# Kernel tuning notes

Hardware: AMD Instinct MI355X
Metric: run time of the kernel (lower is better)

The kernel has to match this reference:

```python
import jax, jax.numpy as jnp
import numpy as np

N_NODE = 50000
N_EDGE = 1600000
D_NODE = 64
D_EDGE = 32
D_OUT = 32
D_IN = 2 * D_NODE + D_EDGE  # 160
D_HID = 2 * D_IN            # 320


def setup_inputs() -> dict:
    key = jax.random.key(0)
    k = jax.random.split(key, 8)
    nodes = jax.random.normal(k[0], (N_NODE, D_NODE), dtype=jnp.float32)
    edges = jax.random.normal(k[1], (N_EDGE, D_EDGE), dtype=jnp.float32)
    senders = jax.random.randint(k[2], (N_EDGE,), 0, N_NODE, dtype=jnp.int64)
    receivers = jax.random.randint(k[3], (N_EDGE,), 0, N_NODE, dtype=jnp.int64)
    # Kaiming-ish scaled linear weights
    W1 = jax.random.normal(k[4], (D_IN, D_HID), dtype=jnp.float32) / np.sqrt(D_IN)
    b1 = jnp.zeros((D_HID,), dtype=jnp.float32)
    W2 = jax.random.normal(k[5], (D_HID, D_OUT), dtype=jnp.float32) / np.sqrt(D_HID)
    b2 = jnp.zeros((D_OUT,), dtype=jnp.float32)
    return {"nodes": nodes, "edges": edges, "senders": senders,
            "receivers": receivers, "W1": W1, "b1": b1, "W2": W2, "b2": b2}


def reference(nodes, edges, senders, receivers, W1, b1, W2, b2):
    # gather sender/receiver node feats, concat with edge feats: [n_edge, 2*d_node+d_edge]
    feats = jnp.concatenate([nodes[senders], nodes[receivers], edges], axis=-1)
    h = jax.nn.sigmoid(feats @ W1 + b1)   # [n_edge, 2*d]
    new_edges = h @ W2 + b2               # [n_edge, d_edge_out]
    return new_edges
```

## Files before the change

### kernel.cpp

```cpp
#include <hip/hip_runtime.h>

typedef unsigned short u16;
typedef short bf8 __attribute__((ext_vector_type(8)));
typedef float f4 __attribute__((ext_vector_type(4)));

#define N_EDGE   1600000
#define NTILE    50000
#define BLOCKS   256
#define WAVES    12
#define NTHREADS (WAVES * 64)
#define SLOTS    (BLOCKS * WAVES)

#define WS_W2_OFF   51200
#define WS_B1_OFF   61440
#define WS_STATIC_B 124160
#define SMEM_INT4   7760

__device__ __forceinline__ u16 f2bf(float x) {
  union { float f; unsigned u; } v; v.f = x;
  unsigned r = v.u + 0x7FFFu + ((v.u >> 16) & 1u);
  return (u16)(r >> 16);
}

__device__ __forceinline__ unsigned pk2(float lo, float hi) {
  unsigned r;
  asm("v_cvt_pk_bf16_f32 %0, %1, %2" : "=v"(r) : "v"(lo), "v"(hi));
  return r;
}

union bfu { uint4 u; bf8 v; };

__device__ __forceinline__ bf8 cvt8r(const float* __restrict__ s) {
  const float4 v0 = *(const float4*)s;
  const float4 v1 = *(const float4*)(s + 4);
  bfu o;
  o.u.x = pk2(v0.x, v0.y); o.u.y = pk2(v0.z, v0.w);
  o.u.z = pk2(v1.x, v1.y); o.u.w = pk2(v1.z, v1.w);
  return o.v;
}

__device__ __forceinline__ bf8 cvt8r_nt(const float* __restrict__ s) {
  const f4 v0 = __builtin_nontemporal_load((const f4*)s);
  const f4 v1 = __builtin_nontemporal_load((const f4*)(s + 4));
  bfu o;
  o.u.x = pk2(v0[0], v0[1]); o.u.y = pk2(v0[2], v0[3]);
  o.u.z = pk2(v1[0], v1[1]); o.u.w = pk2(v1[2], v1[3]);
  return o.v;
}

__global__ void prep_kernel(const float* __restrict__ nodes,
                            const float* __restrict__ W1,
                            const float* __restrict__ b1,
                            const float* __restrict__ W2,
                            u16* __restrict__ w1t,
                            u16* __restrict__ w2t,
                            float* __restrict__ b1t,
                            u16* __restrict__ nodes_bf) {
  const int b = blockIdx.x, t = threadIdx.x;
  if (b < 200) {
    const int i = b * 256 + t;
    const int j = i & 7, lane = (i >> 3) & 63, f = i >> 9;
    const int kk = f % 5, sub = (f / 5) & 1, p = f / 10;
    const int g = lane >> 4, l15 = lane & 15;
    const int k = 32 * kk + 8 * g + j;
    const int hcol = 32 * p + 8 * (l15 >> 2) + 4 * sub + (l15 & 3);
    w1t[i] = f2bf(-1.44269504f * W1[k * 320 + hcol]);
  } else if (b < 240) {
    const int i = (b - 200) * 256 + t;
    const int j = i & 7, lane = (i >> 3) & 63, f = i >> 9;
    const int am = f & 1, p = f >> 1;
    const int g = lane >> 4, l15 = lane & 15;
    w2t[i] = f2bf(W2[(32 * p + 8 * g + j) * 32 + 16 * am + l15]);
  } else if (b == 240) {
    for (int i = t; i < 320; i += 256) {
      const int af = i >> 4, row = i & 15;
      const int hcol = 32 * (af >> 1) + 8 * (row >> 2) + 4 * (af & 1) + (row & 3);
      b1t[i] = -1.44269504f * b1[hcol];
    }
  } else {
    const int i = (b - 241) * 256 + t;
    const float4 v = ((const float4*)nodes)[i];
    ushort4 o;
    o.x = f2bf(v.x); o.y = f2bf(v.y); o.z = f2bf(v.z); o.w = f2bf(v.w);
    ((ushort4*)nodes_bf)[i] = o;
  }
}

__launch_bounds__(NTHREADS, 3)
__global__ void edge_mlp(const float* __restrict__ edges,
                         const int*   __restrict__ senders,
                         const int*   __restrict__ receivers,
                         const float* __restrict__ nodes_f,
                         const u16*   __restrict__ nodes_bf,
                         const int4*  __restrict__ wsrc,
                         const float* __restrict__ b2,
                         float* __restrict__ out,
                         int use_bf) {
  __shared__ __align__(16) int4 smem4[SMEM_INT4];
  const u16*   w1s = (const u16*)smem4;
  const u16*   w2s = w1s + WS_W2_OFF;
  const float* b1s = (const float*)(w1s + WS_B1_OFF);

  for (int i = threadIdx.x; i < SMEM_INT4; i += NTHREADS) smem4[i] = wsrc[i];
  __syncthreads();

  const int tid = threadIdx.x;
  const int lane = tid & 63;
  const int wid  = tid >> 6;
  const int l15  = lane & 15;
  const int g    = lane >> 4;

  f4 b2v[2];
  b2v[0] = *(const f4*)(b2 + 4 * g);
  b2v[1] = *(const f4*)(b2 + 16 + 4 * g);

  for (int t = blockIdx.x * WAVES + wid; t < NTILE; t += SLOTS) {
    const int e0 = t * 32;

    int es[2], er[2];
    es[0] = senders[e0 + l15];        es[1] = senders[e0 + 16 + l15];
    er[0] = receivers[e0 + l15];      er[1] = receivers[e0 + 16 + l15];

    bf8 bf[5][2];
    #pragma unroll
    for (int ef = 0; ef < 2; ++ef) {
      if (use_bf) {
        const u16* sb = nodes_bf + es[ef] * 64;
        const u16* rb = nodes_bf + er[ef] * 64;
        bf[0][ef] = *(const bf8*)(sb + 8 * g);
        bf[1][ef] = *(const bf8*)(sb + 32 + 8 * g);
        bf[2][ef] = *(const bf8*)(rb + 8 * g);
        bf[3][ef] = *(const bf8*)(rb + 32 + 8 * g);
      } else {
        const float* sb = nodes_f + es[ef] * 64;
        const float* rb = nodes_f + er[ef] * 64;
        bf[0][ef] = cvt8r(sb + 8 * g);
        bf[1][ef] = cvt8r(sb + 32 + 8 * g);
        bf[2][ef] = cvt8r(rb + 8 * g);
        bf[3][ef] = cvt8r(rb + 32 + 8 * g);
      }
      bf[4][ef] = cvt8r_nt(edges + (e0 + 16 * ef + l15) * 32 + 8 * g);
    }

    f4 acc2[2][2];
    acc2[0][0] = b2v[0]; acc2[0][1] = b2v[0];
    acc2[1][0] = b2v[1]; acc2[1][1] = b2v[1];

    #pragma unroll 2
    for (int p = 0; p < 10; ++p) {
      f4 h[2][2];
      #pragma unroll
      for (int sub = 0; sub < 2; ++sub) {
        const int af = 2 * p + sub;
        const f4 binit = *(const f4*)(b1s + af * 16 + 4 * g);
        h[sub][0] = binit;
        h[sub][1] = binit;
        #pragma unroll
        for (int kk = 0; kk < 5; ++kk) {
          const bf8 a = *(const bf8*)(w1s + ((p * 10 + sub * 5 + kk) * 64 + lane) * 8);
          h[sub][0] = __builtin_amdgcn_mfma_f32_16x16x32_bf16(a, bf[kk][0], h[sub][0], 0, 0, 0);
          h[sub][1] = __builtin_amdgcn_mfma_f32_16x16x32_bf16(a, bf[kk][1], h[sub][1], 0, 0, 0);
        }
      }
      bf8 pb[2];
      #pragma unroll
      for (int ef = 0; ef < 2; ++ef) {
        f4 s0, s1;
        #pragma unroll
        for (int r = 0; r < 4; ++r) {
          s0[r] = __builtin_amdgcn_rcpf(1.0f + __builtin_amdgcn_exp2f(h[0][ef][r]));
          s1[r] = __builtin_amdgcn_rcpf(1.0f + __builtin_amdgcn_exp2f(h[1][ef][r]));
        }
        bfu o;
        o.u.x = pk2(s0[0], s0[1]); o.u.y = pk2(s0[2], s0[3]);
        o.u.z = pk2(s1[0], s1[1]); o.u.w = pk2(s1[2], s1[3]);
        pb[ef] = o.v;
      }
      #pragma unroll
      for (int am = 0; am < 2; ++am) {
        const bf8 wa = *(const bf8*)(w2s + ((p * 2 + am) * 64 + lane) * 8);
        acc2[am][0] = __builtin_amdgcn_mfma_f32_16x16x32_bf16(wa, pb[0], acc2[am][0], 0, 0, 0);
        acc2[am][1] = __builtin_amdgcn_mfma_f32_16x16x32_bf16(wa, pb[1], acc2[am][1], 0, 0, 0);
      }
    }

    #pragma unroll
    for (int am = 0; am < 2; ++am)
      #pragma unroll
      for (int ef = 0; ef < 2; ++ef)
        __builtin_nontemporal_store(acc2[am][ef],
            (f4*)(out + (e0 + 16 * ef + l15) * 32 + 16 * am + 4 * g));
  }
}

extern "C" void kernel_launch(void* const* d_in, const int* in_sizes, int n_in,
                              void* d_out, int out_size, void* d_ws, size_t ws_size,
                              hipStream_t stream) {
  const float* nodes     = (const float*)d_in[0];
  const float* edges     = (const float*)d_in[1];
  const int*   senders   = (const int*)d_in[2];
  const int*   receivers = (const int*)d_in[3];
  const float* W1        = (const float*)d_in[4];
  const float* b1        = (const float*)d_in[5];
  const float* W2        = (const float*)d_in[6];
  const float* b2        = (const float*)d_in[7];
  float* out             = (float*)d_out;

  u16*   w1t      = (u16*)d_ws;
  u16*   w2t      = w1t + WS_W2_OFF;
  float* b1t      = (float*)(w1t + WS_B1_OFF);
  u16*   nodes_bf = (u16*)((char*)d_ws + WS_STATIC_B);
  const int use_bf = (ws_size >= (size_t)(WS_STATIC_B + 6400000)) ? 1 : 0;

  const int prep_blocks = use_bf ? (241 + 3125) : 241;
  prep_kernel<<<prep_blocks, 256, 0, stream>>>(nodes, W1, b1, W2, w1t, w2t, b1t, nodes_bf);
  edge_mlp<<<BLOCKS, NTHREADS, 0, stream>>>(edges, senders, receivers, nodes, nodes_bf,
                                            (const int4*)d_ws, b2, out, use_bf);
}
```

Measured before the change: 231.4 us.

## Software-pipeline layer-1 MFMA with sigmoid/layer-2 and use library bf16 convert

Restructures the hidden-chunk loop into a two-stage software pipeline. The next chunk's layer-1 MFMAs are issued before the sigmoid and layer-2 MFMAs of the current chunk, so transcendental VALU work can overlap matrix-core latency. The inline-asm packed bf16 convert is also replaced with the HIP library __float2bfloat16, which may produce more instructions than the single packed convert. The double-buffered accumulators raise register pressure under the 3-blocks-per-CU launch bound.

```diff
diff --git a/kernel.cpp b/kernel.cpp
--- a/kernel.cpp
+++ b/kernel.cpp
@@ -1,4 +1,5 @@
 #include <hip/hip_runtime.h>
+#include <hip/hip_bf16.h>
 
 typedef unsigned short u16;
 typedef short bf8 __attribute__((ext_vector_type(8)));
@@ -23,9 +24,10 @@
 }
 
 __device__ __forceinline__ unsigned pk2(float lo, float hi) {
-  unsigned r;
-  asm("v_cvt_pk_bf16_f32 %0, %1, %2" : "=v"(r) : "v"(lo), "v"(hi));
-  return r;
+  union { __hip_bfloat16 b[2]; unsigned u; } o;
+  o.b[0] = __float2bfloat16(lo);
+  o.b[1] = __float2bfloat16(hi);
+  return o.u;
 }
 
 union bfu { uint4 u; bf8 v; };
@@ -86,6 +88,45 @@
   }
 }
 
+#define G1_STAGE(P, H00, H01, H10, H11)                                          \
+  {                                                                              \
+    const f4 bi0 = *(const f4*)(b1s + (2 * (P) + 0) * 16 + 4 * g);               \
+    const f4 bi1 = *(const f4*)(b1s + (2 * (P) + 1) * 16 + 4 * g);               \
+    H00 = bi0; H01 = bi0; H10 = bi1; H11 = bi1;                                  \
+    _Pragma("unroll")                                                            \
+    for (int kk = 0; kk < 5; ++kk) {                                             \
+      const bf8 a0 = *(const bf8*)(w1s + (((P) * 10 + kk) * 64 + lane) * 8);     \
+      const bf8 a1 = *(const bf8*)(w1s + (((P) * 10 + 5 + kk) * 64 + lane) * 8); \
+      H00 = __builtin_amdgcn_mfma_f32_16x16x32_bf16(a0, bf[kk][0], H00, 0, 0, 0);\
+      H01 = __builtin_amdgcn_mfma_f32_16x16x32_bf16(a0, bf[kk][1], H01, 0, 0, 0);\
+      H10 = __builtin_amdgcn_mfma_f32_16x16x32_bf16(a1, bf[kk][0], H10, 0, 0, 0);\
+      H11 = __builtin_amdgcn_mfma_f32_16x16x32_bf16(a1, bf[kk][1], H11, 0, 0, 0);\
+    }                                                                            \
+  }
+
+#define SIG_G2(P, H00, H01, H10, H11)                                            \
+  {                                                                              \
+    f4 s00, s01, s10, s11;                                                       \
+    _Pragma("unroll")                                                            \
+    for (int r = 0; r < 4; ++r) {                                                \
+      s00[r] = __builtin_amdgcn_rcpf(1.0f + __builtin_amdgcn_exp2f(H00[r]));     \
+      s01[r] = __builtin_amdgcn_rcpf(1.0f + __builtin_amdgcn_exp2f(H01[r]));     \
+      s10[r] = __builtin_amdgcn_rcpf(1.0f + __builtin_amdgcn_exp2f(H10[r]));     \
+      s11[r] = __builtin_amdgcn_rcpf(1.0f + __builtin_amdgcn_exp2f(H11[r]));     \
+    }                                                                            \
+    bfu o0, o1;                                                                  \
+    o0.u.x = pk2(s00[0], s00[1]); o0.u.y = pk2(s00[2], s00[3]);                  \
+    o0.u.z = pk2(s10[0], s10[1]); o0.u.w = pk2(s10[2], s10[3]);                  \
+    o1.u.x = pk2(s01[0], s01[1]); o1.u.y = pk2(s01[2], s01[3]);                  \
+    o1.u.z = pk2(s11[0], s11[1]); o1.u.w = pk2(s11[2], s11[3]);                  \
+    const bf8 wa0 = *(const bf8*)(w2s + (((P) * 2 + 0) * 64 + lane) * 8);        \
+    const bf8 wa1 = *(const bf8*)(w2s + (((P) * 2 + 1) * 64 + lane) * 8);        \
+    a2_00 = __builtin_amdgcn_mfma_f32_16x16x32_bf16(wa0, o0.v, a2_00, 0, 0, 0);  \
+    a2_01 = __builtin_amdgcn_mfma_f32_16x16x32_bf16(wa0, o1.v, a2_01, 0, 0, 0);  \
+    a2_10 = __builtin_amdgcn_mfma_f32_16x16x32_bf16(wa1, o0.v, a2_10, 0, 0, 0);  \
+    a2_11 = __builtin_amdgcn_mfma_f32_16x16x32_bf16(wa1, o1.v, a2_11, 0, 0, 0);  \
+  }
+
 __launch_bounds__(NTHREADS, 3)
 __global__ void edge_mlp(const float* __restrict__ edges,
                          const int*   __restrict__ senders,
@@ -142,54 +183,23 @@
       bf[4][ef] = cvt8r_nt(edges + (e0 + 16 * ef + l15) * 32 + 8 * g);
     }
 
-    f4 acc2[2][2];
-    acc2[0][0] = b2v[0]; acc2[0][1] = b2v[0];
-    acc2[1][0] = b2v[1]; acc2[1][1] = b2v[1];
-
-    #pragma unroll 2
-    for (int p = 0; p < 10; ++p) {
-      f4 h[2][2];
-      #pragma unroll
-      for (int sub = 0; sub < 2; ++sub) {
-        const int af = 2 * p + sub;
-        const f4 binit = *(const f4*)(b1s + af * 16 + 4 * g);
-        h[sub][0] = binit;
-        h[sub][1] = binit;
-        #pragma unroll
-        for (int kk = 0; kk < 5; ++kk) {
-          const bf8 a = *(const bf8*)(w1s + ((p * 10 + sub * 5 + kk) * 64 + lane) * 8);
-          h[sub][0] = __builtin_amdgcn_mfma_f32_16x16x32_bf16(a, bf[kk][0], h[sub][0], 0, 0, 0);
-          h[sub][1] = __builtin_amdgcn_mfma_f32_16x16x32_bf16(a, bf[kk][1], h[sub][1], 0, 0, 0);
-        }
-      }
-      bf8 pb[2];
-      #pragma unroll
-      for (int ef = 0; ef < 2; ++ef) {
-        f4 s0, s1;
-        #pragma unroll
-        for (int r = 0; r < 4; ++r) {
-          s0[r] = __builtin_amdgcn_rcpf(1.0f + __builtin_amdgcn_exp2f(h[0][ef][r]));
-          s1[r] = __builtin_amdgcn_rcpf(1.0f + __builtin_amdgcn_exp2f(h[1][ef][r]));
-        }
-        bfu o;
-        o.u.x = pk2(s0[0], s0[1]); o.u.y = pk2(s0[2], s0[3]);
-        o.u.z = pk2(s1[0], s1[1]); o.u.w = pk2(s1[2], s1[3]);
-        pb[ef] = o.v;
-      }
-      #pragma unroll
-      for (int am = 0; am < 2; ++am) {
-        const bf8 wa = *(const bf8*)(w2s + ((p * 2 + am) * 64 + lane) * 8);
-        acc2[am][0] = __builtin_amdgcn_mfma_f32_16x16x32_bf16(wa, pb[0], acc2[am][0], 0, 0, 0);
-        acc2[am][1] = __builtin_amdgcn_mfma_f32_16x16x32_bf16(wa, pb[1], acc2[am][1], 0, 0, 0);
-      }
+    f4 a2_00 = b2v[0], a2_01 = b2v[0];
+    f4 a2_10 = b2v[1], a2_11 = b2v[1];
+
+    f4 hA00, hA01, hA10, hA11, hB00, hB01, hB10, hB11;
+    G1_STAGE(0, hA00, hA01, hA10, hA11);
+    #pragma unroll 1
+    for (int pp = 0; pp < 5; ++pp) {
+      G1_STAGE(2 * pp + 1, hB00, hB01, hB10, hB11);
+      SIG_G2(2 * pp, hA00, hA01, hA10, hA11);
+      if (pp < 4) G1_STAGE(2 * pp + 2, hA00, hA01, hA10, hA11);
+      SIG_G2(2 * pp + 1, hB00, hB01, hB10, hB11);
     }
 
-    #pragma unroll
-    for (int am = 0; am < 2; ++am)
-      #pragma unroll
-      for (int ef = 0; ef < 2; ++ef)
-        __builtin_nontemporal_store(acc2[am][ef],
-            (f4*)(out + (e0 + 16 * ef + l15) * 32 + 16 * am + 4 * g));
+    __builtin_nontemporal_store(a2_00, (f4*)(out + (e0 + l15) * 32 + 4 * g));
+    __builtin_nontemporal_store(a2_01, (f4*)(out + (e0 + 16 + l15) * 32 + 4 * g));
+    __builtin_nontemporal_store(a2_10, (f4*)(out + (e0 + l15) * 32 + 16 + 4 * g));
+    __builtin_nontemporal_store(a2_11, (f4*)(out + (e0 + 16 + l15) * 32 + 16 + 4 * g));
   }
 }
 
```

Result: slower. 305.6 us (+32.1%).
